# Kernel tuning notes

Hardware: AMD Instinct MI355X
Metric: run time of the kernel (lower is better)

The kernel has to match this reference:

```python
import jax, jax.numpy as jnp
import numpy as np

D = 1024
H = 16
HD = D // H  # 64
LN_EPS = 1e-5


def _layernorm(x, w, b):
    m = jnp.mean(x, axis=-1, keepdims=True)
    v = jnp.mean(jnp.square(x - m), axis=-1, keepdims=True)
    return (x - m) * jax.lax.rsqrt(v + LN_EPS) * w + b


def _attention(x, w_qkv, b_qkv, w_proj, b_proj):
    # x: [B, S, D]. Block-diagonal mask == attention within each sequence,
    # so batched per-sequence attention is exactly equivalent to packed fmha.
    B, S, _ = x.shape
    qkv = x @ w_qkv + b_qkv                      # [B, S, 3D]
    q, k, v = jnp.split(qkv, 3, axis=-1)
    q = q.reshape(B, S, H, HD)
    k = k.reshape(B, S, H, HD)
    v = v.reshape(B, S, H, HD)
    scale = 1.0 / jnp.sqrt(jnp.asarray(HD, dtype=x.dtype))
    scores = jnp.einsum('bqhd,bkhd->bhqk', q, k) * scale  # [B, H, S, S]
    probs = jax.nn.softmax(scores, axis=-1)
    out = jnp.einsum('bhqk,bkhd->bqhd', probs, v).reshape(B, S, D)
    return out @ w_proj + b_proj


def _block(x, w_qkv, b_qkv, w_proj, b_proj, ln1_w, ln1_b,
           w_fc1, b_fc1, w_fc2, b_fc2, ln2_w, ln2_b, gamma1, gamma2):
    # x = x + ls1(attn(norm1(x)))
    x = x + gamma1 * _attention(_layernorm(x, ln1_w, ln1_b), w_qkv, b_qkv, w_proj, b_proj)
    # x = x + ls2(mlp(norm2(x)))
    h = _layernorm(x, ln2_w, ln2_b)
    h = jax.nn.gelu(h @ w_fc1 + b_fc1, approximate=False) @ w_fc2 + b_fc2
    return x + gamma2 * h


def setup_inputs() -> dict:
    key = jax.random.key(0)
    ks = jax.random.split(key, 8)
    s = 0.02
    return {
        'x1': jax.random.normal(ks[0], (8, 1024, D), jnp.float32),
        'x2': jax.random.normal(ks[1], (8, 512, D), jnp.float32),
        'w_qkv': jax.random.normal(ks[2], (D, 3 * D), jnp.float32) * s,
        'b_qkv': jnp.zeros((3 * D,), jnp.float32),
        'w_proj': jax.random.normal(ks[3], (D, D), jnp.float32) * s,
        'b_proj': jnp.zeros((D,), jnp.float32),
        'ln1_w': jnp.ones((D,), jnp.float32),
        'ln1_b': jnp.zeros((D,), jnp.float32),
        'ln2_w': jnp.ones((D,), jnp.float32),
        'ln2_b': jnp.zeros((D,), jnp.float32),
        'w_fc1': jax.random.normal(ks[4], (D, 4 * D), jnp.float32) * s,
        'b_fc1': jnp.zeros((4 * D,), jnp.float32),
        'w_fc2': jax.random.normal(ks[5], (4 * D, D), jnp.float32) * s,
        'b_fc2': jnp.zeros((D,), jnp.float32),
        'gamma1': jnp.full((D,), 1e-5, jnp.float32),  # LayerScale init_values
        'gamma2': jnp.full((D,), 1e-5, jnp.float32),
    }


def reference(x1, x2, w_qkv, b_qkv, w_proj, b_proj, ln1_w, ln1_b,
              ln2_w, ln2_b, w_fc1, b_fc1, w_fc2, b_fc2, gamma1, gamma2):
    params = (w_qkv, b_qkv, w_proj, b_proj, ln1_w, ln1_b,
              w_fc1, b_fc1, w_fc2, b_fc2, ln2_w, ln2_b, gamma1, gamma2)
    y1 = _block(x1, *params)
    y2 = _block(x2, *params)
    return (y1, y2)
```

## Files before the change

kernel.cpp:

```cpp
#include <hip/hip_runtime.h>
#include <cstddef>


typedef __bf16 b16x8 __attribute__((ext_vector_type(8)));
typedef float f32x4 __attribute__((ext_vector_type(4)));
typedef unsigned short u16x8 __attribute__((ext_vector_type(8)));
typedef unsigned short u16x4 __attribute__((ext_vector_type(4)));
typedef float f32x4v __attribute__((ext_vector_type(4)));

__device__ __forceinline__ unsigned short f2bf(float f) {
    unsigned int u = __builtin_bit_cast(unsigned int, f);
    return (unsigned short)((u + 0x7fffu + ((u >> 16) & 1u)) >> 16);
}
__device__ __forceinline__ unsigned short f2bf_trunc(float f) {
    return (unsigned short)(__builtin_bit_cast(unsigned int, f) >> 16);
}

__device__ __forceinline__ float exp2_f(float x) {
#if defined(__has_builtin)
#if __has_builtin(__builtin_amdgcn_exp2f)
    return __builtin_amdgcn_exp2f(x);
#else
    return exp2f(x);
#endif
#else
    return exp2f(x);
#endif
}

#define AS1C(p) ((const __attribute__((address_space(1))) void*)(p))
#define AS3(p)  ((__attribute__((address_space(3))) void*)(p))
#define FENCE() asm volatile("" ::: "memory")

__global__ __launch_bounds__(256) void wtrans_k(const float* __restrict__ in,
                                                unsigned short* __restrict__ out,
                                                int K, int N) {
    __shared__ float tile[32][33];
    int n0 = blockIdx.x << 5, k0 = blockIdx.y << 5;
    int tx = threadIdx.x & 31;
    int ty = threadIdx.x >> 5;
#pragma unroll
    for (int j = 0; j < 4; ++j)
        tile[ty + j * 8][tx] = in[(size_t)(k0 + ty + j * 8) * N + n0 + tx];
    __syncthreads();
#pragma unroll
    for (int j = 0; j < 4; ++j)
        out[(size_t)(n0 + ty + j * 8) * K + k0 + tx] = f2bf(tile[tx][ty + j * 8]);
}

__global__ __launch_bounds__(256) void vtrans_k(const unsigned short* __restrict__ qkv,
                                                unsigned short* __restrict__ vT) {
    __shared__ unsigned short tile[32][40];
    int tok0 = blockIdx.x << 5, c0 = blockIdx.y << 5;
    int tx = threadIdx.x & 31, ty = threadIdx.x >> 5;
#pragma unroll
    for (int j = 0; j < 4; ++j)
        tile[ty + j * 8][tx] = qkv[(size_t)(tok0 + ty + j * 8) * 3072 + 2048 + c0 + tx];
    __syncthreads();
#pragma unroll
    for (int j = 0; j < 4; ++j)
        vT[(size_t)(c0 + ty + j * 8) * 12288 + tok0 + tx] = tile[tx][ty + j * 8];
}

__global__ __launch_bounds__(256) void ln_k(const float* __restrict__ srcA,
                                            const float* __restrict__ srcB, int split,
                                            const float* __restrict__ w,
                                            const float* __restrict__ b,
                                            unsigned short* __restrict__ out) {
    int row = blockIdx.x;
    const float* src = (row < split) ? srcA + (size_t)row * 1024
                                     : srcB + (size_t)(row - split) * 1024;
    int t = threadIdx.x;
    f32x4v v = *(const f32x4v*)(src + t * 4);
    float s = v[0] + v[1] + v[2] + v[3];
    float s2 = v[0] * v[0] + v[1] * v[1] + v[2] * v[2] + v[3] * v[3];
#pragma unroll
    for (int off = 1; off < 64; off <<= 1) {
        s += __shfl_xor(s, off);
        s2 += __shfl_xor(s2, off);
    }
    __shared__ float red[8];
    int wv4 = t >> 6;
    if ((t & 63) == 0) { red[wv4 * 2] = s; red[wv4 * 2 + 1] = s2; }
    __syncthreads();
    s = red[0] + red[2] + red[4] + red[6];
    s2 = red[1] + red[3] + red[5] + red[7];
    float mean = s * (1.0f / 1024.0f);
    float var = s2 * (1.0f / 1024.0f) - mean * mean;
    float rstd = rsqrtf(var + 1e-5f);
    f32x4v wv = *(const f32x4v*)(w + t * 4);
    f32x4v bv = *(const f32x4v*)(b + t * 4);
    u16x4 ov;
#pragma unroll
    for (int j = 0; j < 4; ++j) ov[j] = f2bf((v[j] - mean) * rstd * wv[j] + bv[j]);
    *(u16x4*)(out + (size_t)row * 1024 + t * 4) = ov;
}

template <int BM, int K, int NN, int EPI>
__global__ __launch_bounds__(512, 1) void gemm3_k(
    const unsigned short* __restrict__ A, const unsigned short* __restrict__ BT,
    const float* __restrict__ bias, const float* __restrict__ scale,
    const float* __restrict__ rx1, const float* __restrict__ rx2,
    float* __restrict__ outf, unsigned short* __restrict__ outb) {
    constexpr int NT = K / 64;
    constexpr int ntn = NN >> 8;
    constexpr int GA = BM / 64;
    constexpr int NFR = BM / 32;
    constexpr int HALF = NFR / 2;
    constexpr int ABUF = BM * 128;
    constexpr int STRIDE = ABUF + 32768;
    __shared__ char lds[2 * STRIDE];
    const int t = threadIdx.x;
    const int lane = t & 63, w = t >> 6, lr = lane & 15, lg = lane >> 4;
    const int wm = w >> 2, wn = w & 3;
    const int nwg = gridDim.x;
    const int bid = blockIdx.x;
    const int swz = (bid & 7) * (nwg >> 3) + (bid >> 3);
    const int m0 = (swz / ntn) * BM;
    const int n0 = (swz % ntn) << 8;

    const int srow = t >> 3;
    const int scol = ((t & 7) ^ (srow & 7)) * 8;
    const unsigned short* ga = A + (size_t)(m0 + srow) * K + scol;
    const unsigned short* gb = BT + (size_t)(n0 + srow) * K + scol;

    f32x4 acc[NFR][4] = {};
    b16x8 af[HALF][2], b01[2][2], b23[2][2];

    auto ISSUE_A = [&](int tile, int g) {
        char* dst = lds + (tile & 1) * STRIDE + g * 8192 + t * 16;
        __builtin_amdgcn_global_load_lds(AS1C(ga + (size_t)(g * 64) * K + tile * 64),
                                         AS3(dst), 16, 0, 0);
    };
    auto ISSUE_B = [&](int tile, int g) {
        char* dst = lds + (tile & 1) * STRIDE + ABUF + g * 8192 + t * 16;
        __builtin_amdgcn_global_load_lds(AS1C(gb + (size_t)(g * 64) * K + tile * 64),
                                         AS3(dst), 16, 0, 0);
    };

    const int cs0 = (lg ^ (lr & 7)) * 16;
    const int cs1 = ((4 + lg) ^ (lr & 7)) * 16;

    auto RD_A = [&](const char* buf, int mg) {
#pragma unroll
        for (int mi = 0; mi < HALF; ++mi) {
            const char* p = buf + (wm * (BM / 2) + (mg + mi) * 16 + lr) * 128;
            af[mi][0] = *(const b16x8*)(p + cs0);
            af[mi][1] = *(const b16x8*)(p + cs1);
        }
    };
    auto RD_B = [&](const char* buf, b16x8 (*bf)[2], int ng) {
#pragma unroll
        for (int ni = 0; ni < 2; ++ni) {
            const char* p = buf + ABUF + (wn * 64 + (ng + ni) * 16 + lr) * 128;
            bf[ni][0] = *(const b16x8*)(p + cs0);
            bf[ni][1] = *(const b16x8*)(p + cs1);
        }
    };
    auto MM = [&](int mg, b16x8 (*bf)[2], int ng) {
        __builtin_amdgcn_s_setprio(1);
#pragma unroll
        for (int kk = 0; kk < 2; ++kk)
#pragma unroll
            for (int mi = 0; mi < HALF; ++mi)
#pragma unroll
                for (int ni = 0; ni < 2; ++ni)
                    acc[mg + mi][ng + ni] = __builtin_amdgcn_mfma_f32_16x16x32_bf16(
                        af[mi][kk], bf[ni][kk], acc[mg + mi][ng + ni], 0, 0, 0);
        __builtin_amdgcn_s_setprio(0);
    };
    auto WAIT_GA = [&]() {
        if constexpr (GA == 4) asm volatile("s_waitcnt vmcnt(4)" ::: "memory");
        else                   asm volatile("s_waitcnt vmcnt(3)" ::: "memory");
    };

#pragma unroll
    for (int g = 0; g < GA; ++g) ISSUE_A(0, g);
#pragma unroll
    for (int g = 0; g < 4; ++g) ISSUE_B(0, g);
#pragma unroll
    for (int g = 0; g < GA; ++g) ISSUE_A(1, g);
    WAIT_GA();
    __builtin_amdgcn_s_barrier();
    FENCE();

    for (int kt = 0; kt < NT; ++kt) {
        const char* buf = lds + (kt & 1) * STRIDE;
        RD_A(buf, 0); RD_B(buf, b01, 0);
        if (kt + 1 < NT) { ISSUE_B(kt + 1, 0); ISSUE_B(kt + 1, 1); }
        __builtin_amdgcn_s_barrier(); FENCE();
        MM(0, b01, 0);
        __builtin_amdgcn_s_barrier(); FENCE();
        RD_B(buf, b23, 2);
        if (kt + 1 < NT) { ISSUE_B(kt + 1, 2); ISSUE_B(kt + 1, 3); }
        __builtin_amdgcn_s_barrier(); FENCE();
        MM(0, b23, 2);
        __builtin_amdgcn_s_barrier(); FENCE();
        RD_A(buf, HALF);
        __builtin_amdgcn_s_barrier(); FENCE();
        MM(HALF, b23, 2);
        __builtin_amdgcn_s_barrier(); FENCE();
        if (kt + 2 < NT) {
#pragma unroll
            for (int g = 0; g < GA; ++g) ISSUE_A(kt + 2, g);
        }
        __builtin_amdgcn_s_barrier(); FENCE();
        MM(HALF, b01, 0);
        if (kt + 1 < NT) {
            if (kt + 2 < NT) WAIT_GA();
            else             asm volatile("s_waitcnt vmcnt(0)" ::: "memory");
            __builtin_amdgcn_s_barrier(); FENCE();
        }
    }

    if (EPI == 0 || EPI == 2) {
        __syncthreads();
        char* clb = lds;
        const int rl0 = wm * (BM / 2) + lg * 4;
        const int cl0 = wn * 64 + lr;
#pragma unroll
        for (int n = 0; n < 4; ++n) {
            const int col_l = cl0 + n * 16;
            const float bval = bias[n0 + col_l];
            const int colByte = col_l * 2;
            const int within = colByte & 15;
            const int chunk = colByte >> 4;
#pragma unroll
            for (int m = 0; m < NFR; ++m) {
#pragma unroll
                for (int r = 0; r < 4; ++r) {
                    float c = acc[m][n][r] + bval;
                    if (EPI == 2) {
                        float u = c * (c * c * 0.044715f + 1.0f) * 1.5957691216057308f;
                        c = c * __builtin_amdgcn_rcpf(1.0f + __expf(-u));
                    }
                    const int row_l = rl0 + m * 16 + r;
                    *(unsigned short*)(clb + row_l * 512 +
                                       (((chunk ^ (row_l & 7)) << 4) | within)) = f2bf(c);
                }
            }
        }
        __syncthreads();
#pragma unroll
        for (int it = 0; it < BM / 16; ++it) {
            int idx = it * 512 + t;
            int row = idx >> 5, ch = idx & 31;
            u16x8 v = *(const u16x8*)(clb + row * 512 + ((ch ^ (row & 7)) << 4));
            *(u16x8*)(outb + (size_t)(m0 + row) * NN + n0 + ch * 8) = v;
        }
    } else {
        const int rbase = m0 + wm * (BM / 2) + lg * 4;
        const int cbase = n0 + wn * 64 + lr;
#pragma unroll
        for (int n = 0; n < 4; ++n) {
            int col = cbase + n * 16;
            float bval = bias[col];
            float sval = scale[col];
#pragma unroll
            for (int m = 0; m < NFR; ++m) {
                int row = rbase + m * 16;
#pragma unroll
                for (int r = 0; r < 4; ++r) {
                    float c = acc[m][n][r] + bval;
                    size_t idx = (size_t)(row + r) * NN + col;
                    if (EPI == 1) {
                        float xv = (row + r < 8192) ? rx1[idx] : rx2[idx - (size_t)8192 * 1024];
                        outf[idx] = xv + sval * c;
                    } else {
                        outf[idx] += sval * c;
                    }
                }
            }
        }
    }
}

__global__ __launch_bounds__(512) void attn_k(const unsigned short* __restrict__ qkv,
                                              const unsigned short* __restrict__ vT,
                                              unsigned short* __restrict__ aout) {
    __shared__ char sK[2][8192];
    __shared__ char sV[2][8192];
    __shared__ unsigned short sP[8][16 * 72];
    const int xcd = blockIdx.x & 7;
    const int idx = blockIdx.x >> 3;
    int seq0, S, h, qt;
    if (idx < 128) {
        h = idx & 15; qt = idx >> 4; seq0 = xcd << 10; S = 1024;
    } else {
        int j = idx - 128;
        h = j & 15; qt = j >> 4; seq0 = 8192 + (xcd << 9); S = 512;
    }
    int t = threadIdx.x, lane = t & 63, w = t >> 6, lr = lane & 15, lg = lane >> 4;
    int tok0 = seq0 + qt * 128;
    const size_t hoff = (size_t)h * 64;

    const int srow = t >> 3;
    const int sc = ((t & 7) ^ (srow & 7)) * 8;
    const unsigned short* kg = qkv + (size_t)(seq0 + srow) * 3072 + 1024 + hoff + sc;
    const unsigned short* vg = vT + (size_t)(hoff + srow) * 12288 + seq0 + sc;

    b16x8 aq0, aq1;
    {
        const unsigned short* qb = qkv + (size_t)(tok0 + w * 16 + lr) * 3072 + hoff;
        aq0 = *(const b16x8*)(qb + lg * 8);
        aq1 = *(const b16x8*)(qb + 32 + lg * 8);
    }

    auto STAGE = [&](int kt) {
        int slot = kt & 1;
        __builtin_amdgcn_global_load_lds(AS1C(kg + (size_t)(kt << 6) * 3072),
                                         AS3(sK[slot] + t * 16), 16, 0, 0);
        __builtin_amdgcn_global_load_lds(AS1C(vg + (kt << 6)),
                                         AS3(sV[slot] + t * 16), 16, 0, 0);
    };

    const int swz0 = (lg ^ (lr & 7)) * 16;
    const int swz1 = ((4 + lg) ^ (lr & 7)) * 16;
    const float SC = 0.18033688f;

    float lsum[4] = {0.f, 0.f, 0.f, 0.f};
    f32x4 o[4] = {};
    unsigned short* sPw = sP[w];
    const int nkv = S >> 6;

    auto QK = [&](int kt, f32x4 (&s)[4]) {
        const char* kb = sK[kt & 1];
#pragma unroll
        for (int n = 0; n < 4; ++n) {
            const char* kr = kb + (n * 16 + lr) * 128;
            b16x8 bk0 = *(const b16x8*)(kr + swz0);
            b16x8 bk1 = *(const b16x8*)(kr + swz1);
            f32x4 z = {};
            z = __builtin_amdgcn_mfma_f32_16x16x32_bf16(aq0, bk0, z, 0, 0, 0);
            z = __builtin_amdgcn_mfma_f32_16x16x32_bf16(aq1, bk1, z, 0, 0, 0);
            s[n] = z * SC;
        }
    };
    auto SM = [&](f32x4 (&s)[4], b16x8& a0, b16x8& a1) {
        float p[4][4];
#pragma unroll
        for (int n = 0; n < 4; ++n)
#pragma unroll
            for (int r = 0; r < 4; ++r)
                p[n][r] = exp2_f(s[n][r]);
#pragma unroll
        for (int r = 0; r < 4; ++r)
            lsum[r] += (p[0][r] + p[1][r]) + (p[2][r] + p[3][r]);
#pragma unroll
        for (int r = 0; r < 4; ++r)
#pragma unroll
            for (int n = 0; n < 4; ++n)
                sPw[(lg * 4 + r) * 72 + n * 16 + lr] = f2bf_trunc(p[n][r]);
        a0 = *(const b16x8*)(&sPw[lr * 72 + lg * 8]);
        a1 = *(const b16x8*)(&sPw[lr * 72 + 32 + lg * 8]);
    };

    STAGE(0);
    if (nkv > 1) STAGE(1);
    asm volatile("s_waitcnt vmcnt(0)" ::: "memory");
    __builtin_amdgcn_s_barrier();
    FENCE();
    f32x4 s0[4];
    QK(0, s0);
    b16x8 ap0, ap1;
    SM(s0, ap0, ap1);

    for (int kt = 0; kt < nkv; ++kt) {
        const char* vb = sV[kt & 1];
        b16x8 bv0[4], bv1[4];
#pragma unroll
        for (int n = 0; n < 4; ++n) {
            const char* vr = vb + (n * 16 + lr) * 128;
            bv0[n] = *(const b16x8*)(vr + swz0);
            bv1[n] = *(const b16x8*)(vr + swz1);
        }
        f32x4 s2[4];
        if (kt + 1 < nkv) QK(kt + 1, s2);
        asm volatile("s_waitcnt lgkmcnt(0)" ::: "memory");
        __builtin_amdgcn_s_barrier();
        FENCE();
        if (kt + 2 < nkv) STAGE(kt + 2);
#pragma unroll
        for (int n = 0; n < 4; ++n) {
            o[n] = __builtin_amdgcn_mfma_f32_16x16x32_bf16(ap0, bv0[n], o[n], 0, 0, 0);
            o[n] = __builtin_amdgcn_mfma_f32_16x16x32_bf16(ap1, bv1[n], o[n], 0, 0, 0);
        }
        if (kt + 1 < nkv) {
            SM(s2, ap0, ap1);
            asm volatile("s_waitcnt vmcnt(0)" ::: "memory");
            __builtin_amdgcn_s_barrier();
            FENCE();
        }
    }
#pragma unroll
    for (int r = 0; r < 4; ++r) {
        lsum[r] += __shfl_xor(lsum[r], 1);
        lsum[r] += __shfl_xor(lsum[r], 2);
        lsum[r] += __shfl_xor(lsum[r], 4);
        lsum[r] += __shfl_xor(lsum[r], 8);
    }
    __syncthreads();
    char* ob = sK[0];
#pragma unroll
    for (int r = 0; r < 4; ++r) {
        float inv = __builtin_amdgcn_rcpf(lsum[r]);
        const int row_l = w * 16 + lg * 4 + r;
#pragma unroll
        for (int n = 0; n < 4; ++n) {
            const int colByte = (n * 16 + lr) * 2;
            *(unsigned short*)(ob + row_l * 128 +
                               ((((colByte >> 4) ^ (row_l & 7)) << 4) | (colByte & 15))) =
                f2bf(o[n][r] * inv);
        }
    }
    __syncthreads();
#pragma unroll
    for (int it = 0; it < 2; ++it) {
        int idx2 = it * 512 + t;
        int row = idx2 >> 3, ch = idx2 & 7;
        u16x8 v = *(const u16x8*)(ob + row * 128 + ((ch ^ (row & 7)) << 4));
        *(u16x8*)(aout + (size_t)(tok0 + row) * 1024 + hoff + ch * 8) = v;
    }
}

extern "C" void kernel_launch(void* const* d_in, const int* in_sizes, int n_in,
                              void* d_out, int out_size, void* d_ws, size_t ws_size,
                              hipStream_t stream) {
    const float* x1     = (const float*)d_in[0];
    const float* x2     = (const float*)d_in[1];
    const float* w_qkv  = (const float*)d_in[2];
    const float* b_qkv  = (const float*)d_in[3];
    const float* w_proj = (const float*)d_in[4];
    const float* b_proj = (const float*)d_in[5];
    const float* ln1w   = (const float*)d_in[6];
    const float* ln1b   = (const float*)d_in[7];
    const float* ln2w   = (const float*)d_in[8];
    const float* ln2b   = (const float*)d_in[9];
    const float* w_fc1  = (const float*)d_in[10];
    const float* b_fc1  = (const float*)d_in[11];
    const float* w_fc2  = (const float*)d_in[12];
    const float* b_fc2  = (const float*)d_in[13];
    const float* gamma1 = (const float*)d_in[14];
    const float* gamma2 = (const float*)d_in[15];
    float* out = (float*)d_out;
    char* ws = (char*)d_ws;

    unsigned short* wqkvT  = (unsigned short*)(ws);
    unsigned short* wprojT = (unsigned short*)(ws + 6291456);
    unsigned short* wfc1T  = (unsigned short*)(ws + 8388608);
    unsigned short* wfc2T  = (unsigned short*)(ws + 16777216);
    unsigned short* lnbuf  = (unsigned short*)(ws + 25165824);
    unsigned short* qkvbuf = (unsigned short*)(ws + 50331648);
    unsigned short* attnbuf= (unsigned short*)(ws + 125829120);
    unsigned short* actbuf = (unsigned short*)(ws + 50331648);
    unsigned short* vTbuf  = lnbuf;

    wtrans_k<<<dim3(96, 32), 256, 0, stream>>>(w_qkv, wqkvT, 1024, 3072);
    wtrans_k<<<dim3(32, 32), 256, 0, stream>>>(w_proj, wprojT, 1024, 1024);
    wtrans_k<<<dim3(128, 32), 256, 0, stream>>>(w_fc1, wfc1T, 1024, 4096);
    wtrans_k<<<dim3(32, 128), 256, 0, stream>>>(w_fc2, wfc2T, 4096, 1024);
    ln_k<<<12288, 256, 0, stream>>>(x1, x2, 8192, ln1w, ln1b, lnbuf);
    gemm3_k<192, 1024, 3072, 0><<<768, 512, 0, stream>>>(lnbuf, wqkvT, b_qkv, nullptr,
                                                         nullptr, nullptr, nullptr, qkvbuf);
    vtrans_k<<<dim3(384, 32), 256, 0, stream>>>(qkvbuf, vTbuf);
    attn_k<<<1536, 512, 0, stream>>>(qkvbuf, vTbuf, attnbuf);
    gemm3_k<192, 1024, 1024, 1><<<256, 512, 0, stream>>>(attnbuf, wprojT, b_proj, gamma1,
                                                         x1, x2, out, nullptr);
    ln_k<<<12288, 256, 0, stream>>>(out, out + (size_t)8192 * 1024, 8192, ln2w, ln2b, lnbuf);
    gemm3_k<256, 1024, 4096, 2><<<768, 512, 0, stream>>>(lnbuf, wfc1T, b_fc1, nullptr,
                                                         nullptr, nullptr, nullptr, actbuf);
    gemm3_k<192, 4096, 1024, 3><<<256, 512, 0, stream>>>(actbuf, wfc2T, b_fc2, gamma2,
                                                         nullptr, nullptr, out, nullptr);
}
```

Baseline: 503.4 us.

## Double attention query tile per block to 256 rows for K/V reuse

Each attention block now handles 256 query rows, with each wave owning two 16-row groups, instead of 128. Every K/V tile staged in LDS therefore feeds twice as many MFMAs, which halves K/V global traffic and the number of blocks. LDS is merged into one buffer and the P scratch is enlarged to hold both groups. The trade-off is more registers per thread (launch_bounds 512,4 is added), half as many blocks, and therefore less parallelism.

```diff
diff --git a/kernel.cpp b/kernel.cpp
--- a/kernel.cpp
+++ b/kernel.cpp
@@ -275,23 +275,24 @@
     }
 }
 
-__global__ __launch_bounds__(512) void attn_k(const unsigned short* __restrict__ qkv,
-                                              const unsigned short* __restrict__ vT,
-                                              unsigned short* __restrict__ aout) {
-    __shared__ char sK[2][8192];
-    __shared__ char sV[2][8192];
-    __shared__ unsigned short sP[8][16 * 72];
+__global__ __launch_bounds__(512, 4) void attn_k(const unsigned short* __restrict__ qkv,
+                                                 const unsigned short* __restrict__ vT,
+                                                 unsigned short* __restrict__ aout) {
+    __shared__ char sbuf[32768 + 8 * 32 * 72 * 2];
+    char* sKb = sbuf;
+    char* sVb = sbuf + 16384;
+    unsigned short* sP = (unsigned short*)(sbuf + 32768);
     const int xcd = blockIdx.x & 7;
     const int idx = blockIdx.x >> 3;
     int seq0, S, h, qt;
-    if (idx < 128) {
+    if (idx < 64) {
         h = idx & 15; qt = idx >> 4; seq0 = xcd << 10; S = 1024;
     } else {
-        int j = idx - 128;
+        int j = idx - 64;
         h = j & 15; qt = j >> 4; seq0 = 8192 + (xcd << 9); S = 512;
     }
     int t = threadIdx.x, lane = t & 63, w = t >> 6, lr = lane & 15, lg = lane >> 4;
-    int tok0 = seq0 + qt * 128;
+    int tok0 = seq0 + qt * 256;
     const size_t hoff = (size_t)h * 64;
 
     const int srow = t >> 3;
@@ -299,60 +300,70 @@
     const unsigned short* kg = qkv + (size_t)(seq0 + srow) * 3072 + 1024 + hoff + sc;
     const unsigned short* vg = vT + (size_t)(hoff + srow) * 12288 + seq0 + sc;
 
-    b16x8 aq0, aq1;
-    {
-        const unsigned short* qb = qkv + (size_t)(tok0 + w * 16 + lr) * 3072 + hoff;
-        aq0 = *(const b16x8*)(qb + lg * 8);
-        aq1 = *(const b16x8*)(qb + 32 + lg * 8);
+    b16x8 aq[2][2];
+#pragma unroll
+    for (int g = 0; g < 2; ++g) {
+        const unsigned short* qb = qkv + (size_t)(tok0 + w * 32 + g * 16 + lr) * 3072 + hoff;
+        aq[g][0] = *(const b16x8*)(qb + lg * 8);
+        aq[g][1] = *(const b16x8*)(qb + 32 + lg * 8);
     }
 
     auto STAGE = [&](int kt) {
         int slot = kt & 1;
         __builtin_amdgcn_global_load_lds(AS1C(kg + (size_t)(kt << 6) * 3072),
-                                         AS3(sK[slot] + t * 16), 16, 0, 0);
+                                         AS3(sKb + slot * 8192 + t * 16), 16, 0, 0);
         __builtin_amdgcn_global_load_lds(AS1C(vg + (kt << 6)),
-                                         AS3(sV[slot] + t * 16), 16, 0, 0);
+                                         AS3(sVb + slot * 8192 + t * 16), 16, 0, 0);
     };
 
     const int swz0 = (lg ^ (lr & 7)) * 16;
     const int swz1 = ((4 + lg) ^ (lr & 7)) * 16;
     const float SC = 0.18033688f;
 
-    float lsum[4] = {0.f, 0.f, 0.f, 0.f};
-    f32x4 o[4] = {};
-    unsigned short* sPw = sP[w];
+    float lsum[2][4] = {};
+    f32x4 o[2][4] = {};
+    unsigned short* sPw = sP + w * 32 * 72;
     const int nkv = S >> 6;
 
-    auto QK = [&](int kt, f32x4 (&s)[4]) {
-        const char* kb = sK[kt & 1];
+    auto QK = [&](int kt, f32x4 (&s)[2][4]) {
+        const char* kb = sKb + (kt & 1) * 8192;
 #pragma unroll
         for (int n = 0; n < 4; ++n) {
             const char* kr = kb + (n * 16 + lr) * 128;
             b16x8 bk0 = *(const b16x8*)(kr + swz0);
             b16x8 bk1 = *(const b16x8*)(kr + swz1);
-            f32x4 z = {};
-            z = __builtin_amdgcn_mfma_f32_16x16x32_bf16(aq0, bk0, z, 0, 0, 0);
-            z = __builtin_amdgcn_mfma_f32_16x16x32_bf16(aq1, bk1, z, 0, 0, 0);
-            s[n] = z * SC;
-        }
-    };
-    auto SM = [&](f32x4 (&s)[4], b16x8& a0, b16x8& a1) {
-        float p[4][4];
-#pragma unroll
-        for (int n = 0; n < 4; ++n)
+#pragma unroll
+            for (int g = 0; g < 2; ++g) {
+                f32x4 z = {};
+                z = __builtin_amdgcn_mfma_f32_16x16x32_bf16(aq[g][0], bk0, z, 0, 0, 0);
+                z = __builtin_amdgcn_mfma_f32_16x16x32_bf16(aq[g][1], bk1, z, 0, 0, 0);
+                s[g][n] = z * SC;
+            }
+        }
+    };
+    auto SM = [&](f32x4 (&s)[2][4], b16x8 (&ap)[2][2]) {
+#pragma unroll
+        for (int g = 0; g < 2; ++g) {
+            float p[4][4];
+#pragma unroll
+            for (int n = 0; n < 4; ++n)
+#pragma unroll
+                for (int r = 0; r < 4; ++r)
+                    p[n][r] = exp2_f(s[g][n][r]);
 #pragma unroll
             for (int r = 0; r < 4; ++r)
-                p[n][r] = exp2_f(s[n][r]);
-#pragma unroll
-        for (int r = 0; r < 4; ++r)
-            lsum[r] += (p[0][r] + p[1][r]) + (p[2][r] + p[3][r]);
-#pragma unroll
-        for (int r = 0; r < 4; ++r)
-#pragma unroll
-            for (int n = 0; n < 4; ++n)
-                sPw[(lg * 4 + r) * 72 + n * 16 + lr] = f2bf_trunc(p[n][r]);
-        a0 = *(const b16x8*)(&sPw[lr * 72 + lg * 8]);
-        a1 = *(const b16x8*)(&sPw[lr * 72 + 32 + lg * 8]);
+                lsum[g][r] += (p[0][r] + p[1][r]) + (p[2][r] + p[3][r]);
+#pragma unroll
+            for (int r = 0; r < 4; ++r)
+#pragma unroll
+                for (int n = 0; n < 4; ++n)
+                    sPw[(g * 16 + lg * 4 + r) * 72 + n * 16 + lr] = f2bf_trunc(p[n][r]);
+        }
+#pragma unroll
+        for (int g = 0; g < 2; ++g) {
+            ap[g][0] = *(const b16x8*)(&sPw[(g * 16 + lr) * 72 + lg * 8]);
+            ap[g][1] = *(const b16x8*)(&sPw[(g * 16 + lr) * 72 + 32 + lg * 8]);
+        }
     };
 
     STAGE(0);
@@ -360,13 +371,13 @@
     asm volatile("s_waitcnt vmcnt(0)" ::: "memory");
     __builtin_amdgcn_s_barrier();
     FENCE();
-    f32x4 s0[4];
+    f32x4 s0[2][4];
     QK(0, s0);
-    b16x8 ap0, ap1;
-    SM(s0, ap0, ap1);
+    b16x8 ap[2][2];
+    SM(s0, ap);
 
     for (int kt = 0; kt < nkv; ++kt) {
-        const char* vb = sV[kt & 1];
+        const char* vb = sVb + (kt & 1) * 8192;
         b16x8 bv0[4], bv1[4];
 #pragma unroll
         for (int n = 0; n < 4; ++n) {
@@ -374,7 +385,7 @@
             bv0[n] = *(const b16x8*)(vr + swz0);
             bv1[n] = *(const b16x8*)(vr + swz1);
         }
-        f32x4 s2[4];
+        f32x4 s2[2][4];
         if (kt + 1 < nkv) QK(kt + 1, s2);
         asm volatile("s_waitcnt lgkmcnt(0)" ::: "memory");
         __builtin_amdgcn_s_barrier();
@@ -382,40 +393,47 @@
         if (kt + 2 < nkv) STAGE(kt + 2);
 #pragma unroll
         for (int n = 0; n < 4; ++n) {
-            o[n] = __builtin_amdgcn_mfma_f32_16x16x32_bf16(ap0, bv0[n], o[n], 0, 0, 0);
-            o[n] = __builtin_amdgcn_mfma_f32_16x16x32_bf16(ap1, bv1[n], o[n], 0, 0, 0);
+#pragma unroll
+            for (int g = 0; g < 2; ++g) {
+                o[g][n] = __builtin_amdgcn_mfma_f32_16x16x32_bf16(ap[g][0], bv0[n], o[g][n], 0, 0, 0);
+                o[g][n] = __builtin_amdgcn_mfma_f32_16x16x32_bf16(ap[g][1], bv1[n], o[g][n], 0, 0, 0);
+            }
         }
         if (kt + 1 < nkv) {
-            SM(s2, ap0, ap1);
+            SM(s2, ap);
             asm volatile("s_waitcnt vmcnt(0)" ::: "memory");
             __builtin_amdgcn_s_barrier();
             FENCE();
         }
     }
 #pragma unroll
-    for (int r = 0; r < 4; ++r) {
-        lsum[r] += __shfl_xor(lsum[r], 1);
-        lsum[r] += __shfl_xor(lsum[r], 2);
-        lsum[r] += __shfl_xor(lsum[r], 4);
-        lsum[r] += __shfl_xor(lsum[r], 8);
-    }
+    for (int g = 0; g < 2; ++g)
+#pragma unroll
+        for (int r = 0; r < 4; ++r) {
+            lsum[g][r] += __shfl_xor(lsum[g][r], 1);
+            lsum[g][r] += __shfl_xor(lsum[g][r], 2);
+            lsum[g][r] += __shfl_xor(lsum[g][r], 4);
+            lsum[g][r] += __shfl_xor(lsum[g][r], 8);
+        }
     __syncthreads();
-    char* ob = sK[0];
-#pragma unroll
-    for (int r = 0; r < 4; ++r) {
-        float inv = __builtin_amdgcn_rcpf(lsum[r]);
-        const int row_l = w * 16 + lg * 4 + r;
-#pragma unroll
-        for (int n = 0; n < 4; ++n) {
-            const int colByte = (n * 16 + lr) * 2;
-            *(unsigned short*)(ob + row_l * 128 +
-                               ((((colByte >> 4) ^ (row_l & 7)) << 4) | (colByte & 15))) =
-                f2bf(o[n][r] * inv);
-        }
-    }
+    char* ob = sbuf;
+#pragma unroll
+    for (int g = 0; g < 2; ++g)
+#pragma unroll
+        for (int r = 0; r < 4; ++r) {
+            float inv = __builtin_amdgcn_rcpf(lsum[g][r]);
+            const int row_l = w * 32 + g * 16 + lg * 4 + r;
+#pragma unroll
+            for (int n = 0; n < 4; ++n) {
+                const int colByte = (n * 16 + lr) * 2;
+                *(unsigned short*)(ob + row_l * 128 +
+                                   ((((colByte >> 4) ^ (row_l & 7)) << 4) | (colByte & 15))) =
+                    f2bf(o[g][n][r] * inv);
+            }
+        }
     __syncthreads();
 #pragma unroll
-    for (int it = 0; it < 2; ++it) {
+    for (int it = 0; it < 4; ++it) {
         int idx2 = it * 512 + t;
         int row = idx2 >> 3, ch = idx2 & 7;
         u16x8 v = *(const u16x8*)(ob + row * 128 + ((ch ^ (row & 7)) << 4));
@@ -463,7 +481,7 @@
     gemm3_k<192, 1024, 3072, 0><<<768, 512, 0, stream>>>(lnbuf, wqkvT, b_qkv, nullptr,
                                                          nullptr, nullptr, nullptr, qkvbuf);
     vtrans_k<<<dim3(384, 32), 256, 0, stream>>>(qkvbuf, vTbuf);
-    attn_k<<<1536, 512, 0, stream>>>(qkvbuf, vTbuf, attnbuf);
+    attn_k<<<768, 512, 0, stream>>>(qkvbuf, vTbuf, attnbuf);
     gemm3_k<192, 1024, 1024, 1><<<256, 512, 0, stream>>>(attnbuf, wprojT, b_proj, gamma1,
                                                          x1, x2, out, nullptr);
     ln_k<<<12288, 256, 0, stream>>>(out, out + (size_t)8192 * 1024, 8192, ln2w, ln2b, lnbuf);
```

Result: slower. 524.8 us (+4.3%).
